# Optimization experiments

Hardware: AMD Instinct MI355X
Metric: run time of the kernel (lower is better)

## Reference

```python
import jax, jax.numpy as jnp
import numpy as np

N_NODES = 100000
N_EDGES = 1600000
NFEAT = 256
NHID = 128
NCLASS = 8


def setup_inputs() -> dict:
    key = jax.random.key(0)
    k1, k2, k3, k4, k5 = jax.random.split(key, 5)
    x = jax.random.normal(k1, (N_NODES, NFEAT), dtype=jnp.float32)
    edge_index = jax.random.randint(k2, (2, N_EDGES), 0, N_NODES, dtype=jnp.int64)
    # GCNConv weight (glorot) and bias
    s1 = float(np.sqrt(6.0 / (NFEAT + NHID)))
    W1 = jax.random.uniform(k3, (NFEAT, NHID), dtype=jnp.float32, minval=-s1, maxval=s1)
    b1 = jnp.zeros((NHID,), dtype=jnp.float32)
    # fc Linear (xavier uniform per weights_init, bias zero)
    s2 = float(np.sqrt(6.0 / (NHID + NCLASS)))
    Wfc = jax.random.uniform(k4, (NHID, NCLASS), dtype=jnp.float32, minval=-s2, maxval=s2)
    bfc = jnp.zeros((NCLASS,), dtype=jnp.float32)
    return {"x": x, "edge_index": edge_index, "W1": W1, "b1": b1, "Wfc": Wfc, "bfc": bfc}


def gcn_conv(x, src, dst, W, b, n_nodes):
    # PyG GCNConv: h = X W; out_i = sum_j norm_ij * h_j over A+I with sym norm
    h = x @ W  # [N, nhid]
    deg = jax.ops.segment_sum(jnp.ones_like(dst, dtype=h.dtype), dst, num_segments=n_nodes)
    dinv = jnp.where(deg > 0, jax.lax.rsqrt(deg), 0.0)  # deg^{-1/2}
    norm = dinv[src] * dinv[dst]  # [E+N]
    msg = h[src] * norm[:, None]  # gather + scale, [E+N, nhid]
    out = jax.ops.segment_sum(msg, dst, num_segments=n_nodes)
    return out + b


def reference(x, edge_index, W1, b1, Wfc, bfc):
    n = x.shape[0]
    loop = jnp.arange(n, dtype=edge_index.dtype)
    src = jnp.concatenate([edge_index[0], loop])  # add self-loops
    dst = jnp.concatenate([edge_index[1], loop])
    h = gcn_conv(x, src, dst, W1, b1, n)  # GCN_Body (no activation in forward)
    return h @ Wfc + bfc  # fc
```

## Files before the change

### kernel.cpp

```cpp
#include <hip/hip_runtime.h>

#define N_NODES 100000
#define NFEAT 256
#define NHID 128
#define NCLASS 8

#define BSH 8
#define BUCK 256
#define NBUCK ((N_NODES + BUCK - 1) / BUCK)
#define VX 8
#define CAPS 704
#define GSTRIDE (NBUCK * CAPS)
#define CAPB (CAPS * VX)
#define NBLK1 2048
#define OVF_CAP 32768

__global__ __launch_bounds__(512) void init_kernel(const float* __restrict__ W1,
        const float* __restrict__ b1, const float* __restrict__ Wfc,
        const float* __restrict__ bfc, float* __restrict__ WcT,
        float* __restrict__ cvec, int* __restrict__ gcur, int* __restrict__ ovf_cnt) {
    int tid = threadIdx.x;
    if (blockIdx.x == 0) {
        __shared__ float wfs[NHID * NCLASS];
        __shared__ float bs[NHID];
        for (int i = tid; i < NHID * NCLASS; i += 512) wfs[i] = Wfc[i];
        if (tid < NHID) bs[tid] = b1[tid];
        __syncthreads();
        if (tid < NFEAT) {
            float acc[NCLASS] = {};
            for (int h = 0; h < NHID; h++) {
                float w = W1[tid * NHID + h];
                #pragma unroll
                for (int c = 0; c < NCLASS; c++) acc[c] += w * wfs[h * NCLASS + c];
            }
            #pragma unroll
            for (int c = 0; c < NCLASS; c++) WcT[c * NFEAT + tid] = acc[c];
        }
        if (tid < NCLASS) {
            float a = bfc[tid];
            for (int h = 0; h < NHID; h++) a += bs[h] * wfs[h * NCLASS + tid];
            cvec[tid] = a;
        }
    } else {
        int i = (blockIdx.x - 1) * 512 + tid;
        if (i < VX * NBUCK) {
            int g = i / NBUCK;
            int b = i - g * NBUCK;
            gcur[i] = g * GSTRIDE + b * CAPS;
        }
        if (blockIdx.x == 1 && tid == 0) *ovf_cnt = 0;
    }
}

__global__ __launch_bounds__(256) void scat_kernel(const int* __restrict__ esrc,
        const int* __restrict__ edst, int* __restrict__ gcur,
        int* __restrict__ ebufP, int* __restrict__ ovf_cnt,
        int* __restrict__ ovfbuf, int chunk, int nE) {
    __shared__ int h[NBUCK];
    __shared__ int lcur[NBUCK];
    int tid = threadIdx.x;
    int xcc;
    asm volatile("s_getreg_b32 %0, hwreg(HW_REG_XCC_ID)" : "=s"(xcc));
    xcc &= (VX - 1);
    for (int i = tid; i < NBUCK; i += 256) h[i] = 0;
    __syncthreads();
    int e0 = blockIdx.x * chunk;
    int e1 = min(e0 + chunk, nE);
    for (int e = e0 + tid * 4; e + 3 < e1; e += 1024) {
        int4 d = *(const int4*)&edst[e];
        atomicAdd(&h[d.x >> BSH], 1); atomicAdd(&h[d.y >> BSH], 1);
        atomicAdd(&h[d.z >> BSH], 1); atomicAdd(&h[d.w >> BSH], 1);
    }
    int full = e0 + ((e1 - e0) & ~3);
    if (full + tid < e1) atomicAdd(&h[edst[full + tid] >> BSH], 1);
    __syncthreads();
    const int gbase = xcc * GSTRIDE;
    for (int b = tid; b < NBUCK; b += 256) {
        int c = h[b];
        lcur[b] = c ? atomicAdd(&gcur[xcc * NBUCK + b], c) : 0;
    }
    __syncthreads();
    for (int e = e0 + tid * 4; e + 3 < e1; e += 1024) {
        int4 s = *(const int4*)&esrc[e];
        int4 d = *(const int4*)&edst[e];
        int b0 = d.x >> BSH, b1_ = d.y >> BSH, b2 = d.z >> BSH, b3 = d.w >> BSH;
        int p0 = atomicAdd(&lcur[b0], 1);
        int p1 = atomicAdd(&lcur[b1_], 1);
        int p2 = atomicAdd(&lcur[b2], 1);
        int p3 = atomicAdd(&lcur[b3], 1);
        int k0 = (s.x << BSH) | (d.x & (BUCK - 1));
        int k1 = (s.y << BSH) | (d.y & (BUCK - 1));
        int k2 = (s.z << BSH) | (d.z & (BUCK - 1));
        int k3 = (s.w << BSH) | (d.w & (BUCK - 1));
        if (p0 < gbase + b0 * CAPS + CAPS) ebufP[p0] = k0;
        else { int op = atomicAdd(ovf_cnt, 1); if (op < OVF_CAP) { ovfbuf[2*op] = k0; ovfbuf[2*op+1] = b0; } }
        if (p1 < gbase + b1_ * CAPS + CAPS) ebufP[p1] = k1;
        else { int op = atomicAdd(ovf_cnt, 1); if (op < OVF_CAP) { ovfbuf[2*op] = k1; ovfbuf[2*op+1] = b1_; } }
        if (p2 < gbase + b2 * CAPS + CAPS) ebufP[p2] = k2;
        else { int op = atomicAdd(ovf_cnt, 1); if (op < OVF_CAP) { ovfbuf[2*op] = k2; ovfbuf[2*op+1] = b2; } }
        if (p3 < gbase + b3 * CAPS + CAPS) ebufP[p3] = k3;
        else { int op = atomicAdd(ovf_cnt, 1); if (op < OVF_CAP) { ovfbuf[2*op] = k3; ovfbuf[2*op+1] = b3; } }
    }
    if (full + tid < e1) {
        int s = esrc[full + tid], d = edst[full + tid];
        int b = d >> BSH;
        int p = atomicAdd(&lcur[b], 1);
        int k = (s << BSH) | (d & (BUCK - 1));
        if (p < gbase + b * CAPS + CAPS) ebufP[p] = k;
        else { int op = atomicAdd(ovf_cnt, 1); if (op < OVF_CAP) { ovfbuf[2*op] = k; ovfbuf[2*op+1] = b; } }
    }
}

__global__ __launch_bounds__(512) void deg_dinv_kernel(const int* __restrict__ ebufP,
        const int* __restrict__ gcur, const int* __restrict__ ovf_cnt,
        const int* __restrict__ ovfbuf, float* __restrict__ dinv) {
    __shared__ int cnt[BUCK];
    int b = blockIdx.x, tid = threadIdx.x;
    if (tid < BUCK) cnt[tid] = 0;
    __syncthreads();
    #pragma unroll
    for (int g = 0; g < VX; g++) {
        int base = g * GSTRIDE + b * CAPS;
        int end = min(gcur[g * NBUCK + b], base + CAPS);
        int n = end - base;
        const int4* p4 = (const int4*)&ebufP[base];
        int n4 = n >> 2;
        for (int k = tid; k < n4; k += 512) {
            int4 p = p4[k];
            atomicAdd(&cnt[p.x & (BUCK - 1)], 1);
            atomicAdd(&cnt[p.y & (BUCK - 1)], 1);
            atomicAdd(&cnt[p.z & (BUCK - 1)], 1);
            atomicAdd(&cnt[p.w & (BUCK - 1)], 1);
        }
        for (int k = (n4 << 2) + tid; k < n; k += 512)
            atomicAdd(&cnt[ebufP[base + k] & (BUCK - 1)], 1);
    }
    int nov = min(*ovf_cnt, OVF_CAP);
    for (int i = tid; i < nov; i += 512)
        if (ovfbuf[2 * i + 1] == b) atomicAdd(&cnt[ovfbuf[2 * i] & (BUCK - 1)], 1);
    __syncthreads();
    if (tid < BUCK) {
        int node = (b << BSH) + tid;
        if (node < N_NODES) dinv[node] = rsqrtf((float)(cnt[tid] + 1));
    }
}

__global__ __launch_bounds__(256) void z_kernel(const float* __restrict__ X,
                                                const float* __restrict__ WcT,
                                                const float* __restrict__ dinv,
                                                float* __restrict__ Zs, int n) {
    __shared__ float4 wlds[NCLASS * 64];
    int tid = threadIdx.x;
    #pragma unroll
    for (int i = tid; i < NCLASS * 64; i += 256)
        wlds[i] = ((const float4*)WcT)[i];
    __syncthreads();

    const int lane = tid & 63;
    const int sub  = lane & 7;
    const int rsub = lane >> 3;
    const int wid  = (blockIdx.x * 256 + tid) >> 6;
    const int nw   = (gridDim.x * 256) >> 6;
    const int ngroups = (n + 7) >> 3;

    for (int g = wid; g < ngroups; g += nw) {
        int row = g * 8 + rsub;
        bool ok = row < n;
        int r = ok ? row : (n - 1);
        const float4* xr = (const float4*)(X + (long)r * NFEAT);
        float4 xv[8];
        #pragma unroll
        for (int k = 0; k < 8; k++) xv[k] = xr[sub + 8 * k];

        float res = 0.f;
        #pragma unroll
        for (int c = 0; c < NCLASS; c++) {
            float s = 0.f;
            #pragma unroll
            for (int k = 0; k < 8; k++) {
                float4 w = wlds[c * 64 + sub + 8 * k];
                s += xv[k].x * w.x + xv[k].y * w.y + xv[k].z * w.z + xv[k].w * w.w;
            }
            s += __shfl_xor(s, 1);
            s += __shfl_xor(s, 2);
            s += __shfl_xor(s, 4);
            if (sub == c) res = s;
        }
        if (ok) Zs[(long)row * NCLASS + sub] = res * dinv[row];
    }
}

__global__ __launch_bounds__(512) void sort_gather_kernel(
        const float* __restrict__ Zs,
        const int* __restrict__ ebufP,
        const int* __restrict__ gcur,
        const int* __restrict__ ovf_cnt,
        const int* __restrict__ ovfbuf,
        const float* __restrict__ cvec,
        float* __restrict__ out, int n) {
    __shared__ int cnt[BUCK];
    __shared__ int off[BUCK + 1];
    __shared__ int ss[BUCK];
    __shared__ int sorted[CAPB];
    int b = blockIdx.x, tid = threadIdx.x;
    const float4* Zs4 = (const float4*)Zs;
    float4 c0v = ((const float4*)cvec)[0];
    float4 c1v = ((const float4*)cvec)[1];
    int nov = min(*ovf_cnt, OVF_CAP);

    if (tid < BUCK) cnt[tid] = 0;
    __syncthreads();
    #pragma unroll
    for (int g = 0; g < VX; g++) {
        int base = g * GSTRIDE + b * CAPS;
        int end = min(gcur[g * NBUCK + b], base + CAPS);
        int nn = end - base;
        const int4* p4 = (const int4*)&ebufP[base];
        int n4 = nn >> 2;
        for (int k = tid; k < n4; k += 512) {
            int4 p = p4[k];
            atomicAdd(&cnt[p.x & (BUCK - 1)], 1);
            atomicAdd(&cnt[p.y & (BUCK - 1)], 1);
            atomicAdd(&cnt[p.z & (BUCK - 1)], 1);
            atomicAdd(&cnt[p.w & (BUCK - 1)], 1);
        }
        for (int k = (n4 << 2) + tid; k < nn; k += 512)
            atomicAdd(&cnt[ebufP[base + k] & (BUCK - 1)], 1);
    }
    for (int i = tid; i < nov; i += 512)
        if (ovfbuf[2 * i + 1] == b) atomicAdd(&cnt[ovfbuf[2 * i] & (BUCK - 1)], 1);
    __syncthreads();

    int t = (tid < BUCK) ? cnt[tid] : 0;
    if (tid < BUCK) ss[tid] = t;
    __syncthreads();
    for (int o = 1; o < BUCK; o <<= 1) {
        int u = 0;
        if (tid < BUCK && tid >= o) u = ss[tid - o];
        __syncthreads();
        if (tid < BUCK) ss[tid] += u;
        __syncthreads();
    }
    if (tid < BUCK) {
        off[tid] = ss[tid] - t;
        cnt[tid] = ss[tid] - t;
        if (tid == BUCK - 1) off[BUCK] = ss[tid];
    }
    __syncthreads();

    #pragma unroll
    for (int g = 0; g < VX; g++) {
        int base = g * GSTRIDE + b * CAPS;
        int end = min(gcur[g * NBUCK + b], base + CAPS);
        int nn = end - base;
        const int4* p4 = (const int4*)&ebufP[base];
        int n4 = nn >> 2;
        for (int k = tid; k < n4; k += 512) {
            int4 p = p4[k];
            int s0 = atomicAdd(&cnt[p.x & (BUCK - 1)], 1);
            int s1 = atomicAdd(&cnt[p.y & (BUCK - 1)], 1);
            int s2 = atomicAdd(&cnt[p.z & (BUCK - 1)], 1);
            int s3 = atomicAdd(&cnt[p.w & (BUCK - 1)], 1);
            sorted[s0] = p.x >> BSH;
            sorted[s1] = p.y >> BSH;
            sorted[s2] = p.z >> BSH;
            sorted[s3] = p.w >> BSH;
        }
        for (int k = (n4 << 2) + tid; k < nn; k += 512) {
            int p = ebufP[base + k];
            int slot = atomicAdd(&cnt[p & (BUCK - 1)], 1);
            sorted[slot] = p >> BSH;
        }
    }
    for (int i = tid; i < nov; i += 512) {
        if (ovfbuf[2 * i + 1] == b) {
            int p = ovfbuf[2 * i];
            int slot = atomicAdd(&cnt[p & (BUCK - 1)], 1);
            sorted[slot] = p >> BSH;
        }
    }
    __syncthreads();

    int li = tid >> 1;
    int hh = tid & 1;
    int node = (b << BSH) + li;
    if (node < n) {
        int k0 = off[li], k1 = off[li + 1];
        float4 a = Zs4[node * 2 + hh];
        int k = k0;
        for (; k + 1 < k1; k += 2) {
            int s0 = sorted[k], s1 = sorted[k + 1];
            float4 z0 = Zs4[s0 * 2 + hh];
            float4 z1 = Zs4[s1 * 2 + hh];
            a.x += z0.x + z1.x; a.y += z0.y + z1.y;
            a.z += z0.z + z1.z; a.w += z0.w + z1.w;
        }
        if (k < k1) {
            float4 z = Zs4[sorted[k] * 2 + hh];
            a.x += z.x; a.y += z.y; a.z += z.z; a.w += z.w;
        }
        float dd = rsqrtf((float)(k1 - k0 + 1));
        float4 cv = hh ? c1v : c0v;
        float4 o;
        o.x = a.x * dd + cv.x; o.y = a.y * dd + cv.y;
        o.z = a.z * dd + cv.z; o.w = a.w * dd + cv.w;
        ((float4*)out)[node * 2 + hh] = o;
    }
}

extern "C" void kernel_launch(void* const* d_in, const int* in_sizes, int n_in,
                              void* d_out, int out_size, void* d_ws, size_t ws_size,
                              hipStream_t stream) {
    const float* x    = (const float*)d_in[0];
    const int*   eidx = (const int*)d_in[1];
    const float* W1   = (const float*)d_in[2];
    const float* b1   = (const float*)d_in[3];
    const float* Wfc  = (const float*)d_in[4];
    const float* bfc  = (const float*)d_in[5];
    float* out = (float*)d_out;

    const int N = N_NODES;
    const int E = in_sizes[1] / 2;

    const int* esrc = eidx;
    const int* edst = eidx + E;

    float* Zs     = (float*)d_ws;
    float* cvec   = Zs + (long)8 * N;
    float* WcT    = cvec + 8;
    float* dinv   = WcT + NCLASS * NFEAT;
    int*   gcur   = (int*)(dinv + N);
    int*   ovfc   = gcur + VX * NBUCK;
    int*   ovfbuf = ovfc + 4;
    int*   ebufP  = ovfbuf + 2 * OVF_CAP;

    const int chunk = (((E + NBLK1 - 1) / NBLK1) + 3) & ~3;

    init_kernel<<<1 + (VX * NBUCK + 511) / 512, 512, 0, stream>>>(
        W1, b1, Wfc, bfc, WcT, cvec, gcur, ovfc);
    scat_kernel<<<NBLK1, 256, 0, stream>>>(esrc, edst, gcur, ebufP, ovfc, ovfbuf, chunk, E);
    deg_dinv_kernel<<<NBUCK, 512, 0, stream>>>(ebufP, gcur, ovfc, ovfbuf, dinv);
    z_kernel<<<1563, 256, 0, stream>>>(x, WcT, dinv, Zs, N);
    sort_gather_kernel<<<NBUCK, 512, 0, stream>>>(Zs, ebufP, gcur, ovfc, ovfbuf, cvec, out, N);
}
```

Baseline: 239.3 us.

## Restructure z_kernel to stage X tiles in LDS with one row per thread

The X·Wc projection kernel now uses 64-thread blocks. Each block loads a 64-row tile of X into LDS with an XOR swizzle, then each thread computes all 8 class outputs for its own row, with weights read from global memory in a row-major layout. This removes the shuffle reductions and redundant per-class LDS weight reads, and makes the Zs writes vectorized float4 stores. The trade-offs are 64 KB of LDS per block, which limits occupancy, and weight reads that go through cache instead of LDS.

```diff
diff --git a/kernel.cpp b/kernel.cpp
--- a/kernel.cpp
+++ b/kernel.cpp
@@ -14,10 +14,11 @@
 #define CAPB (CAPS * VX)
 #define NBLK1 2048
 #define OVF_CAP 32768
+#define ZROWS 64
 
 __global__ __launch_bounds__(512) void init_kernel(const float* __restrict__ W1,
         const float* __restrict__ b1, const float* __restrict__ Wfc,
-        const float* __restrict__ bfc, float* __restrict__ WcT,
+        const float* __restrict__ bfc, float* __restrict__ Wf,
         float* __restrict__ cvec, int* __restrict__ gcur, int* __restrict__ ovf_cnt) {
     int tid = threadIdx.x;
     if (blockIdx.x == 0) {
@@ -34,7 +35,7 @@
                 for (int c = 0; c < NCLASS; c++) acc[c] += w * wfs[h * NCLASS + c];
             }
             #pragma unroll
-            for (int c = 0; c < NCLASS; c++) WcT[c * NFEAT + tid] = acc[c];
+            for (int c = 0; c < NCLASS; c++) Wf[tid * NCLASS + c] = acc[c];
         }
         if (tid < NCLASS) {
             float a = bfc[tid];
@@ -145,48 +146,41 @@
     }
 }
 
-__global__ __launch_bounds__(256) void z_kernel(const float* __restrict__ X,
-                                                const float* __restrict__ WcT,
-                                                const float* __restrict__ dinv,
-                                                float* __restrict__ Zs, int n) {
-    __shared__ float4 wlds[NCLASS * 64];
-    int tid = threadIdx.x;
-    #pragma unroll
-    for (int i = tid; i < NCLASS * 64; i += 256)
-        wlds[i] = ((const float4*)WcT)[i];
-    __syncthreads();
-
-    const int lane = tid & 63;
-    const int sub  = lane & 7;
-    const int rsub = lane >> 3;
-    const int wid  = (blockIdx.x * 256 + tid) >> 6;
-    const int nw   = (gridDim.x * 256) >> 6;
-    const int ngroups = (n + 7) >> 3;
-
-    for (int g = wid; g < ngroups; g += nw) {
-        int row = g * 8 + rsub;
-        bool ok = row < n;
-        int r = ok ? row : (n - 1);
-        const float4* xr = (const float4*)(X + (long)r * NFEAT);
-        float4 xv[8];
+__global__ __launch_bounds__(64) void z_kernel(const float* __restrict__ X,
+                                               const float* __restrict__ Wf,
+                                               const float* __restrict__ dinv,
+                                               float* __restrict__ Zs, int n) {
+    __shared__ float4 xt[ZROWS * 64];
+    const int l = threadIdx.x;
+    const int base = blockIdx.x * ZROWS;
+
+    #pragma unroll 16
+    for (int i = 0; i < ZROWS; i++) {
+        int r = base + i; if (r >= n) r = n - 1;
+        float4 v = ((const float4*)(X + (long)r * NFEAT))[l];
+        xt[i * 64 + (l ^ (i & 7))] = v;
+    }
+    __syncthreads();
+
+    int row = base + l;
+    bool ok = row < n;
+    float acc[NCLASS] = {};
+    #pragma unroll 4
+    for (int g = 0; g < 64; g++) {
+        float4 x4 = xt[l * 64 + (g ^ (l & 7))];
+        const float* w = Wf + g * 32;
         #pragma unroll
-        for (int k = 0; k < 8; k++) xv[k] = xr[sub + 8 * k];
-
-        float res = 0.f;
-        #pragma unroll
-        for (int c = 0; c < NCLASS; c++) {
-            float s = 0.f;
-            #pragma unroll
-            for (int k = 0; k < 8; k++) {
-                float4 w = wlds[c * 64 + sub + 8 * k];
-                s += xv[k].x * w.x + xv[k].y * w.y + xv[k].z * w.z + xv[k].w * w.w;
-            }
-            s += __shfl_xor(s, 1);
-            s += __shfl_xor(s, 2);
-            s += __shfl_xor(s, 4);
-            if (sub == c) res = s;
-        }
-        if (ok) Zs[(long)row * NCLASS + sub] = res * dinv[row];
+        for (int c = 0; c < NCLASS; c++)
+            acc[c] += x4.x * w[c] + x4.y * w[8 + c]
+                    + x4.z * w[16 + c] + x4.w * w[24 + c];
+    }
+    if (ok) {
+        float dv = dinv[row];
+        float4 o0, o1;
+        o0.x = acc[0] * dv; o0.y = acc[1] * dv; o0.z = acc[2] * dv; o0.w = acc[3] * dv;
+        o1.x = acc[4] * dv; o1.y = acc[5] * dv; o1.z = acc[6] * dv; o1.w = acc[7] * dv;
+        ((float4*)Zs)[(long)row * 2]     = o0;
+        ((float4*)Zs)[(long)row * 2 + 1] = o1;
     }
 }
 
@@ -327,8 +321,8 @@
 
     float* Zs     = (float*)d_ws;
     float* cvec   = Zs + (long)8 * N;
-    float* WcT    = cvec + 8;
-    float* dinv   = WcT + NCLASS * NFEAT;
+    float* Wf     = cvec + 8;
+    float* dinv   = Wf + NFEAT * NCLASS;
     int*   gcur   = (int*)(dinv + N);
     int*   ovfc   = gcur + VX * NBUCK;
     int*   ovfbuf = ovfc + 4;
@@ -337,9 +331,9 @@
     const int chunk = (((E + NBLK1 - 1) / NBLK1) + 3) & ~3;
 
     init_kernel<<<1 + (VX * NBUCK + 511) / 512, 512, 0, stream>>>(
-        W1, b1, Wfc, bfc, WcT, cvec, gcur, ovfc);
+        W1, b1, Wfc, bfc, Wf, cvec, gcur, ovfc);
     scat_kernel<<<NBLK1, 256, 0, stream>>>(esrc, edst, gcur, ebufP, ovfc, ovfbuf, chunk, E);
     deg_dinv_kernel<<<NBUCK, 512, 0, stream>>>(ebufP, gcur, ovfc, ovfbuf, dinv);
-    z_kernel<<<1563, 256, 0, stream>>>(x, WcT, dinv, Zs, N);
+    z_kernel<<<(N + ZROWS - 1) / ZROWS, 64, 0, stream>>>(x, Wf, dinv, Zs, N);
     sort_gather_kernel<<<NBUCK, 512, 0, stream>>>(Zs, ebufP, gcur, ovfc, ovfbuf, cvec, out, N);
 }
```

Result: slower. 252.5 us (+5.5%).
